# Kernel optimization log

Hardware: AMD Instinct MI355X
Metric: run time of the kernel (lower is better)

Reference implementation:

```python
import jax, jax.numpy as jnp
import numpy as np

N_NODES = 100000
N_EDGES = 1600000
N_FEAT = 16
HEADS = 4


def _feast_conv(x, src, dst, U, c, W, b):
    """FeaStConv: q = softmax_h(u^T(x_j - x_i) + c); out_i = mean_j sum_h q_h * (W_h x_j) + b."""
    n = x.shape[0]
    e = src.shape[0]
    xj = x[src]                                   # [E, Fin] gather
    q = jax.nn.softmax(jnp.matmul(xj - x[dst], U) + c, axis=-1)   # [E, H]
    xs = jnp.matmul(xj, W).reshape(e, HEADS, -1)  # [E, H, Fout]
    msg = jnp.einsum('eh,eho->eo', q, xs)         # [E, Fout]
    deg = jax.ops.segment_sum(jnp.ones((e,), x.dtype), dst, num_segments=n)
    agg = jax.ops.segment_sum(msg, dst, num_segments=n)
    return agg / jnp.maximum(deg, 1.0)[:, None] + b


def setup_inputs() -> dict:
    key = jax.random.key(0)
    ks = jax.random.split(key, 32)
    s = 0.1
    d = {
        'x': jax.random.normal(ks[0], (N_NODES, N_FEAT), jnp.float32),
        'edge_index': jax.random.randint(ks[1], (2, N_EDGES), 0, N_NODES, jnp.int32),
        # conv1: 16 -> 16
        'U1': jax.random.normal(ks[2], (N_FEAT, HEADS), jnp.float32) * s,
        'c1': jnp.zeros((HEADS,), jnp.float32),
        'W1': jax.random.normal(ks[3], (N_FEAT, HEADS * 16), jnp.float32) * s,
        'b1': jnp.zeros((16,), jnp.float32),
        # conv2: 16 -> 32
        'U2': jax.random.normal(ks[4], (16, HEADS), jnp.float32) * s,
        'c2': jnp.zeros((HEADS,), jnp.float32),
        'W2': jax.random.normal(ks[5], (16, HEADS * 32), jnp.float32) * s,
        'b2': jnp.zeros((32,), jnp.float32),
        # conv3: 32 -> 64
        'U3': jax.random.normal(ks[6], (32, HEADS), jnp.float32) * s,
        'c3': jnp.zeros((HEADS,), jnp.float32),
        'W3': jax.random.normal(ks[7], (32, HEADS * 64), jnp.float32) * s,
        'b3': jnp.zeros((64,), jnp.float32),
        # linear tail 64->32->16->8->4->1
        'lw1': jax.random.normal(ks[8], (64, 32), jnp.float32) * s,
        'lb1': jnp.zeros((32,), jnp.float32),
        'lw2': jax.random.normal(ks[9], (32, 16), jnp.float32) * s,
        'lb2': jnp.zeros((16,), jnp.float32),
        'lw3': jax.random.normal(ks[10], (16, 8), jnp.float32) * s,
        'lb3': jnp.zeros((8,), jnp.float32),
        'lw4': jax.random.normal(ks[11], (8, 4), jnp.float32) * s,
        'lb4': jnp.zeros((4,), jnp.float32),
        'lw5': jax.random.normal(ks[12], (4, 1), jnp.float32) * s,
        'lb5': jnp.zeros((1,), jnp.float32),
    }
    return d


def reference(x, edge_index, U1, c1, W1, b1, U2, c2, W2, b2, U3, c3, W3, b3,
              lw1, lb1, lw2, lb2, lw3, lb3, lw4, lb4, lw5, lb5):
    src, dst = edge_index[0], edge_index[1]
    h = jax.nn.relu(_feast_conv(x, src, dst, U1, c1, W1, b1))
    h = jax.nn.relu(_feast_conv(h, src, dst, U2, c2, W2, b2))
    h = jax.nn.relu(_feast_conv(h, src, dst, U3, c3, W3, b3))
    # dropout disabled (inference / drop_bool=False): Linear+ReLU tail
    h = jax.nn.relu(jnp.matmul(h, lw1) + lb1)
    h = jax.nn.relu(jnp.matmul(h, lw2) + lb2)
    h = jax.nn.relu(jnp.matmul(h, lw3) + lb3)
    h = jax.nn.relu(jnp.matmul(h, lw4) + lb4)
    return jax.nn.sigmoid(jnp.matmul(h, lw5) + lb5)   # [N, 1]
```

## Files before the change

### kernel.cpp

```cpp
#include <hip/hip_runtime.h>
#include <math.h>

#define N_NODES 100000
#define N_EDGES 1600000
#define HEADS 4
#define NBKT ((N_NODES + 255) / 256)
#define CHUNK_E 4096
#define NCHUNK ((N_EDGES + CHUNK_E - 1) / CHUNK_E)
#define GN ((N_NODES + 255) / 256)
#define SUM_ROWS 16
#define NRB ((NCHUNK + SUM_ROWS - 1) / SUM_ROWS)

typedef unsigned short ushort_t;
typedef unsigned char  uchar_t;

__device__ __forceinline__ ushort_t f2bf(float x) {
    unsigned u = __float_as_uint(x);
    u += 0x7FFF + ((u >> 16) & 1);
    return (ushort_t)(u >> 16);
}
__device__ __forceinline__ float bf2f(ushort_t v) {
    return __uint_as_float(((unsigned)v) << 16);
}
__device__ __forceinline__ void unpack2(unsigned u, float& lo, float& hi) {
    lo = __uint_as_float(u << 16);
    hi = __uint_as_float(u & 0xffff0000u);
}
__device__ __forceinline__ uchar_t f2fp8(float x) {
    if (x <= 0.0f) return 0;
    unsigned u = __float_as_uint(x) + (1u << 19);
    int e = (int)(u >> 23) - 127 + 15;
    if (e <= 0) return 0;
    if (e > 31) return (uchar_t)255;
    return (uchar_t)((e << 3) | ((u >> 20) & 7));
}
__device__ __forceinline__ float fp8d(uchar_t b) {
    unsigned v = (((unsigned)(b >> 3) + 112u) << 23) | ((unsigned)(b & 7) << 20);
    return (b == 0) ? 0.0f : __uint_as_float(v);
}


__global__ __launch_bounds__(256) void bhist_pcast_kernel(
        const int* __restrict__ dst, int* __restrict__ hist_rows,
        const float* __restrict__ x, const float* __restrict__ U,
        float* __restrict__ p, ushort_t* __restrict__ xbf,
        int* __restrict__ bucket_cnt)
{
    __shared__ int h[NBKT];
    if (blockIdx.x < NCHUNK) {
        for (int i = threadIdx.x; i < NBKT; i += 256) h[i] = 0;
        __syncthreads();
        int base = blockIdx.x * CHUNK_E;
        #pragma unroll
        for (int j = 0; j < CHUNK_E / 256; j++) {
            int e = base + j * 256 + threadIdx.x;
            if (e < N_EDGES) atomicAdd(&h[dst[e] >> 8], 1);
        }
        __syncthreads();
        for (int i = threadIdx.x; i < NBKT; i += 256)
            hist_rows[(size_t)blockIdx.x * NBKT + i] = h[i];
    } else if (blockIdx.x < NCHUNK + GN) {
        int n = (blockIdx.x - NCHUNK) * 256 + threadIdx.x;
        if (n >= N_NODES) return;
        float a0 = 0, a1 = 0, a2 = 0, a3 = 0;
        const float* hr = x + (size_t)n * 16;
        float xv[16];
        #pragma unroll
        for (int f = 0; f < 16; f++) {
            xv[f] = hr[f];
            a0 += xv[f] * U[f * 4 + 0];
            a1 += xv[f] * U[f * 4 + 1];
            a2 += xv[f] * U[f * 4 + 2];
            a3 += xv[f] * U[f * 4 + 3];
        }
        *(float4*)(p + (size_t)n * 4) =
            make_float4(__expf(a0), __expf(a1), __expf(a2), __expf(a3));
        #pragma unroll
        for (int j = 0; j < 4; j++) {
            ushort4 u;
            u.x = f2bf(xv[4 * j + 0]); u.y = f2bf(xv[4 * j + 1]);
            u.z = f2bf(xv[4 * j + 2]); u.w = f2bf(xv[4 * j + 3]);
            *(ushort4*)(xbf + (size_t)n * 16 + 4 * j) = u;
        }
    } else {
        for (int i = threadIdx.x; i < NBKT; i += 256) bucket_cnt[i] = 0;
    }
}


__global__ __launch_bounds__(256) void ksum_kernel(const int* __restrict__ hist_rows,
                                                   int* __restrict__ bucket_cnt) {
    int r0 = blockIdx.x * SUM_ROWS;
    int r1 = min(r0 + SUM_ROWS, NCHUNK);
    for (int i = threadIdx.x; i < NBKT; i += 256) {
        int v = 0;
        for (int r = r0; r < r1; r++) v += hist_rows[(size_t)r * NBKT + i];
        if (v) atomicAdd(&bucket_cnt[i], v);
    }
}


__global__ __launch_bounds__(512) void bscan_kernel(const int* __restrict__ bucket_cnt,
                                                    int* __restrict__ bucket_base,
                                                    int* __restrict__ bucket_cursor) {
    __shared__ int tmp[512];
    int i = threadIdx.x;
    int v = (i < NBKT) ? bucket_cnt[i] : 0;
    tmp[i] = v;
    __syncthreads();
    for (int off = 1; off < 512; off <<= 1) {
        int t = (i >= off) ? tmp[i - off] : 0;
        __syncthreads();
        tmp[i] += t;
        __syncthreads();
    }
    int excl = tmp[i] - v;
    if (i < NBKT) { bucket_base[i] = excl; bucket_cursor[i] = excl; }
    if (i == NBKT) bucket_base[NBKT] = N_EDGES;
}


__global__ __launch_bounds__(256) void partition_kernel(const int* __restrict__ src,
                                                        const int* __restrict__ dst,
                                                        int* __restrict__ bucket_cursor,
                                                        int* __restrict__ csr_tmp) {
    constexpr int EPT = CHUNK_E / 256;
    __shared__ int h[NBKT];
    __shared__ int gbase[NBKT];
    __shared__ int rcnt[NBKT];
    for (int i = threadIdx.x; i < NBKT; i += 256) { h[i] = 0; rcnt[i] = 0; }
    __syncthreads();
    int base = blockIdx.x * CHUNK_E;
    int d[EPT], s[EPT];
    #pragma unroll
    for (int j = 0; j < EPT; j++) {
        int e = base + j * 256 + threadIdx.x;
        d[j] = (e < N_EDGES) ? dst[e] : -1;
        s[j] = (e < N_EDGES) ? src[e] : 0;
        if (d[j] >= 0) atomicAdd(&h[d[j] >> 8], 1);
    }
    __syncthreads();
    for (int i = threadIdx.x; i < NBKT; i += 256)
        if (h[i]) gbase[i] = atomicAdd(&bucket_cursor[i], h[i]);
    __syncthreads();
    #pragma unroll
    for (int j = 0; j < EPT; j++) {
        if (d[j] >= 0) {
            int b = d[j] >> 8;
            int r = atomicAdd(&rcnt[b], 1);
            csr_tmp[gbase[b] + r] = ((d[j] & 255) << 20) | s[j];
        }
    }
}


__global__ __launch_bounds__(256) void bucket_build_kernel(const int* __restrict__ bucket_base,
                                                           const int* __restrict__ csr_tmp,
                                                           int* __restrict__ rowptr,
                                                           int* __restrict__ csr_src) {
    __shared__ int cnt[256];
    __shared__ int tscan[256];
    __shared__ int exc[256];
    __shared__ int stage[8192];
    int b = blockIdx.x;
    int rbeg = bucket_base[b], rend = bucket_base[b + 1];
    int sz = rend - rbeg;
    int tid = threadIdx.x;

    cnt[tid] = 0;
    __syncthreads();
    for (int k = rbeg + tid; k < rend; k += 256) atomicAdd(&cnt[csr_tmp[k] >> 20], 1);
    __syncthreads();
    int v = cnt[tid];
    tscan[tid] = v;
    __syncthreads();
    for (int off = 1; off < 256; off <<= 1) {
        int t = (tid >= off) ? tscan[tid - off] : 0;
        __syncthreads();
        tscan[tid] += t;
        __syncthreads();
    }
    int ex = tscan[tid] - v;
    int node = b * 256 + tid;
    if (node < N_NODES) rowptr[node] = rbeg + ex;
    if (b == 0 && tid == 0) rowptr[N_NODES] = N_EDGES;
    exc[tid] = ex;
    cnt[tid] = 0;
    __syncthreads();

    if (sz <= 8192) {
        for (int k = rbeg + tid; k < rend; k += 256) {
            int pk = csr_tmp[k];
            int dl = pk >> 20;
            int r  = atomicAdd(&cnt[dl], 1);
            stage[exc[dl] + r] = pk;
        }
        __syncthreads();
        for (int i = tid; i < sz; i += 256) csr_src[rbeg + i] = stage[i];
    } else {
        for (int k = rbeg + tid; k < rend; k += 256) {
            int pk = csr_tmp[k];
            int dl = pk >> 20;
            int r  = atomicAdd(&cnt[dl], 1);
            csr_src[rbeg + exc[dl] + r] = pk;
        }
    }
}


template<int FIN, int FOUT, int OUT_FP8>
__global__ __launch_bounds__(256) void conv_fused_kernel(
        const int* __restrict__ rowptr, const int* __restrict__ csr_src,
        const float* __restrict__ es, const float* __restrict__ cvec,
        const ushort_t* __restrict__ hprev,
        const float* __restrict__ W,
        const float* __restrict__ b,
        ushort_t* __restrict__ out_bf,
        uchar_t* __restrict__ out_f8,
        const float* __restrict__ Unext,
        float* __restrict__ esnext)
{
    constexpr int LPN   = FIN / 4;
    constexpr int NPB   = 256 / LPN;
    constexpr int CHUNK = 1024;
    constexpr int K     = 4 * FIN;
    constexpr int ZK    = K + 4;
    constexpr int HS    = FOUT + 1;
    constexpr int WSZ   = K * FOUT;
    constexpr int UNION_A = CHUNK * 16 + CHUNK * 4;
    constexpr int UNION_B = NPB * ZK * 4 + NPB * HS * 4;
    constexpr int UNION   = UNION_A > UNION_B ? UNION_A : UNION_B;

    __shared__ int    sbeg[NPB + 1];
    __shared__ __align__(16) float4 pds[NPB];
    __shared__ __align__(16) float  Ws[WSZ];
    __shared__ float  Uloc[FOUT * 4];
    __shared__ __align__(16) char ubuf[UNION];
    float4* qs    = (float4*)ubuf;
    int*    ssrc  = (int*)(ubuf + CHUNK * 16);
    float*  ztile = (float*)ubuf;
    float*  hout  = (float*)(ubuf + NPB * ZK * 4);

    int tid  = threadIdx.x;
    int nloc = tid / LPN;
    int fl   = (tid - nloc * LPN) * 4;
    int n0   = blockIdx.x * NPB;
    int dbase = n0 & 255;

    float ec0 = __expf(cvec[0]), ec1 = __expf(cvec[1]);
    float ec2 = __expf(cvec[2]), ec3 = __expf(cvec[3]);

    for (int i = tid; i <= NPB; i += 256) {
        int idx = n0 + i;
        sbeg[i] = rowptr[idx > N_NODES ? N_NODES : idx];
    }
    for (int i = tid; i < NPB; i += 256) {
        int idx = n0 + i;
        float4 e = *(const float4*)(es + (size_t)(idx < N_NODES ? idx : N_NODES - 1) * 4);
        pds[i] = make_float4(ec0 / e.x, ec1 / e.y, ec2 / e.z, ec3 / e.w);
    }
    for (int i = tid; i < WSZ; i += 256) {
        int f = i / (4 * FOUT);
        int r = i - f * (4 * FOUT);
        int h = r / FOUT;
        int o = r - h * FOUT;
        Ws[(h * FIN + f) * FOUT + o] = W[i];
    }
    for (int i = tid; i < FOUT * 4; i += 256) Uloc[i] = Unext[i];
    __syncthreads();

    int BB = sbeg[0], BE = sbeg[NPB];
    int beg = sbeg[nloc], end = sbeg[nloc + 1];

    float4 acc0 = make_float4(0, 0, 0, 0), acc1 = acc0, acc2 = acc0, acc3 = acc0;

    for (int cbase = BB; cbase < BE; cbase += CHUNK) {
        int cend = min(cbase + CHUNK, BE);
        __syncthreads();
        for (int k = cbase + tid; k < cend; k += 256) {
            int pk = csr_src[k];
            int s  = pk & ((1 << 20) - 1);
            int nl = (pk >> 20) - dbase;
            float4 e  = *(const float4*)(es + (size_t)s * 4);
            float4 ed = pds[nl];
            float w0 = e.x * ed.x;
            float w1 = e.y * ed.y;
            float w2 = e.z * ed.z;
            float w3 = e.w * ed.w;
            float deg = (float)(sbeg[nl + 1] - sbeg[nl]);
            float inv = 1.0f / (fmaxf(deg, 1.0f) * (w0 + w1 + w2 + w3));
            qs[k - cbase]   = make_float4(w0 * inv, w1 * inv, w2 * inv, w3 * inv);
            ssrc[k - cbase] = s;
        }
        __syncthreads();
        int kb = (beg > cbase ? beg : cbase) - cbase;
        int ke = (end < cend ? end : cend) - cbase;
        int k = kb;
        for (; k + 4 <= ke; k += 4) {
            uint2 r[4];
            #pragma unroll
            for (int j = 0; j < 4; j++)
                r[j] = *(const uint2*)(hprev + (size_t)ssrc[k + j] * FIN + fl);
            float xv[4][4];
            #pragma unroll
            for (int j = 0; j < 4; j++) {
                unpack2(r[j].x, xv[j][0], xv[j][1]);
                unpack2(r[j].y, xv[j][2], xv[j][3]);
            }
            #pragma unroll
            for (int j = 0; j < 4; j++) {
                float4 q = qs[k + j];
                acc0.x += q.x * xv[j][0]; acc0.y += q.x * xv[j][1];
                acc0.z += q.x * xv[j][2]; acc0.w += q.x * xv[j][3];
                acc1.x += q.y * xv[j][0]; acc1.y += q.y * xv[j][1];
                acc1.z += q.y * xv[j][2]; acc1.w += q.y * xv[j][3];
                acc2.x += q.z * xv[j][0]; acc2.y += q.z * xv[j][1];
                acc2.z += q.z * xv[j][2]; acc2.w += q.z * xv[j][3];
                acc3.x += q.w * xv[j][0]; acc3.y += q.w * xv[j][1];
                acc3.z += q.w * xv[j][2]; acc3.w += q.w * xv[j][3];
            }
        }
        for (; k < ke; k++) {
            float x0, x1, x2, x3;
            uint2 r = *(const uint2*)(hprev + (size_t)ssrc[k] * FIN + fl);
            unpack2(r.x, x0, x1);
            unpack2(r.y, x2, x3);
            float4 q = qs[k];
            acc0.x += q.x * x0; acc0.y += q.x * x1; acc0.z += q.x * x2; acc0.w += q.x * x3;
            acc1.x += q.y * x0; acc1.y += q.y * x1; acc1.z += q.y * x2; acc1.w += q.y * x3;
            acc2.x += q.z * x0; acc2.y += q.z * x1; acc2.z += q.z * x2; acc2.w += q.z * x3;
            acc3.x += q.w * x0; acc3.y += q.w * x1; acc3.z += q.w * x2; acc3.w += q.w * x3;
        }
    }

    __syncthreads();
    {
        float* zr = ztile + nloc * ZK;
        *(float4*)(zr + 0 * FIN + fl) = acc0;
        *(float4*)(zr + 1 * FIN + fl) = acc1;
        *(float4*)(zr + 2 * FIN + fl) = acc2;
        *(float4*)(zr + 3 * FIN + fl) = acc3;
    }
    __syncthreads();

    constexpr int OQ  = FOUT / 4;
    constexpr int QPT = (NPB * OQ) / 256;
    #pragma unroll
    for (int rq = 0; rq < QPT; rq++) {
        int idx = tid + 256 * rq;
        int j   = idx / OQ;
        int o4  = idx - j * OQ;
        float4 acc = *(const float4*)(b + 4 * o4);
        const float* zr = ztile + j * ZK;
        #pragma unroll 4
        for (int kq = 0; kq < K / 4; kq++) {
            float4 zt = *(const float4*)(zr + 4 * kq);
            #pragma unroll
            for (int jj = 0; jj < 4; jj++) {
                float4 wv = *(const float4*)(Ws + (4 * kq + jj) * FOUT + 4 * o4);
                float s = (&zt.x)[jj];
                acc.x += s * wv.x;
                acc.y += s * wv.y;
                acc.z += s * wv.z;
                acc.w += s * wv.w;
            }
        }
        acc.x = fmaxf(acc.x, 0.0f);
        acc.y = fmaxf(acc.y, 0.0f);
        acc.z = fmaxf(acc.z, 0.0f);
        acc.w = fmaxf(acc.w, 0.0f);
        float* hr = hout + j * HS + 4 * o4;
        hr[0] = acc.x; hr[1] = acc.y; hr[2] = acc.z; hr[3] = acc.w;
        int nn = n0 + j;
        if (nn < N_NODES) {
            if (OUT_FP8) {
                unsigned pk = (unsigned)f2fp8(acc.x) | ((unsigned)f2fp8(acc.y) << 8) |
                              ((unsigned)f2fp8(acc.z) << 16) | ((unsigned)f2fp8(acc.w) << 24);
                *(unsigned*)(out_f8 + (size_t)nn * FOUT + 4 * o4) = pk;
            } else {
                ushort4 u;
                u.x = f2bf(acc.x); u.y = f2bf(acc.y); u.z = f2bf(acc.z); u.w = f2bf(acc.w);
                *(ushort4*)(out_bf + (size_t)nn * FOUT + 4 * o4) = u;
            }
        }
    }

    __syncthreads();
    if (tid < NPB) {
        int nn = n0 + tid;
        if (nn < N_NODES) {
            float a0 = 0, a1 = 0, a2 = 0, a3 = 0;
            const float* hr = hout + tid * HS;
            #pragma unroll
            for (int ff = 0; ff < FOUT; ff++) {
                float xv = hr[ff];
                a0 += xv * Uloc[ff * 4 + 0];
                a1 += xv * Uloc[ff * 4 + 1];
                a2 += xv * Uloc[ff * 4 + 2];
                a3 += xv * Uloc[ff * 4 + 3];
            }
            *(float4*)(esnext + (size_t)nn * 4) =
                make_float4(__expf(a0), __expf(a1), __expf(a2), __expf(a3));
        }
    }
}


template<int FIN>
__global__ __launch_bounds__(256) void zgather_kernel(
        const int* __restrict__ rowptr, const int* __restrict__ csr_src,
        const float* __restrict__ es, const float* __restrict__ cvec,
        const uchar_t* __restrict__ hf8,
        ushort_t* __restrict__ z)
{
    constexpr int LPN   = FIN / 4;
    constexpr int NPB   = 256 / LPN;
    constexpr int CHUNK = 1024;
    __shared__ int    sbeg[NPB + 1];
    __shared__ __align__(16) float4 pds[NPB];
    __shared__ __align__(16) float4 qs[CHUNK];
    __shared__ int    ssrc[CHUNK];

    int tid  = threadIdx.x;
    int nloc = tid / LPN;
    int fl   = (tid - nloc * LPN) * 4;
    int n0   = blockIdx.x * NPB;
    int n    = n0 + nloc;
    int dbase = n0 & 255;

    float ec0 = __expf(cvec[0]), ec1 = __expf(cvec[1]);
    float ec2 = __expf(cvec[2]), ec3 = __expf(cvec[3]);

    for (int i = tid; i <= NPB; i += 256) {
        int idx = n0 + i;
        sbeg[i] = rowptr[idx > N_NODES ? N_NODES : idx];
    }
    for (int i = tid; i < NPB; i += 256) {
        int idx = n0 + i;
        float4 e = *(const float4*)(es + (size_t)(idx < N_NODES ? idx : N_NODES - 1) * 4);
        pds[i] = make_float4(ec0 / e.x, ec1 / e.y, ec2 / e.z, ec3 / e.w);
    }
    __syncthreads();

    int BB = sbeg[0], BE = sbeg[NPB];
    int beg = sbeg[nloc], end = sbeg[nloc + 1];

    float4 acc0 = make_float4(0, 0, 0, 0), acc1 = acc0, acc2 = acc0, acc3 = acc0;

    for (int cbase = BB; cbase < BE; cbase += CHUNK) {
        int cend = min(cbase + CHUNK, BE);
        __syncthreads();
        for (int k = cbase + tid; k < cend; k += 256) {
            int pk = csr_src[k];
            int s  = pk & ((1 << 20) - 1);
            int nl = (pk >> 20) - dbase;
            float4 e  = *(const float4*)(es + (size_t)s * 4);
            float4 ed = pds[nl];
            float w0 = e.x * ed.x;
            float w1 = e.y * ed.y;
            float w2 = e.z * ed.z;
            float w3 = e.w * ed.w;
            float deg = (float)(sbeg[nl + 1] - sbeg[nl]);
            float inv = 1.0f / (fmaxf(deg, 1.0f) * (w0 + w1 + w2 + w3));
            qs[k - cbase]   = make_float4(w0 * inv, w1 * inv, w2 * inv, w3 * inv);
            ssrc[k - cbase] = s;
        }
        __syncthreads();
        int kb = (beg > cbase ? beg : cbase) - cbase;
        int ke = (end < cend ? end : cend) - cbase;
        int k = kb;
        for (; k + 4 <= ke; k += 4) {
            unsigned r[4];
            #pragma unroll
            for (int j = 0; j < 4; j++)
                r[j] = *(const unsigned*)(hf8 + (size_t)ssrc[k + j] * FIN + fl);
            float xv[4][4];
            #pragma unroll
            for (int j = 0; j < 4; j++) {
                xv[j][0] = fp8d((uchar_t)(r[j] & 255));
                xv[j][1] = fp8d((uchar_t)((r[j] >> 8) & 255));
                xv[j][2] = fp8d((uchar_t)((r[j] >> 16) & 255));
                xv[j][3] = fp8d((uchar_t)(r[j] >> 24));
            }
            #pragma unroll
            for (int j = 0; j < 4; j++) {
                float4 q = qs[k + j];
                acc0.x += q.x * xv[j][0]; acc0.y += q.x * xv[j][1];
                acc0.z += q.x * xv[j][2]; acc0.w += q.x * xv[j][3];
                acc1.x += q.y * xv[j][0]; acc1.y += q.y * xv[j][1];
                acc1.z += q.y * xv[j][2]; acc1.w += q.y * xv[j][3];
                acc2.x += q.z * xv[j][0]; acc2.y += q.z * xv[j][1];
                acc2.z += q.z * xv[j][2]; acc2.w += q.z * xv[j][3];
                acc3.x += q.w * xv[j][0]; acc3.y += q.w * xv[j][1];
                acc3.z += q.w * xv[j][2]; acc3.w += q.w * xv[j][3];
            }
        }
        for (; k < ke; k++) {
            unsigned r = *(const unsigned*)(hf8 + (size_t)ssrc[k] * FIN + fl);
            float x0 = fp8d((uchar_t)(r & 255));
            float x1 = fp8d((uchar_t)((r >> 8) & 255));
            float x2 = fp8d((uchar_t)((r >> 16) & 255));
            float x3 = fp8d((uchar_t)(r >> 24));
            float4 q = qs[k];
            acc0.x += q.x * x0; acc0.y += q.x * x1; acc0.z += q.x * x2; acc0.w += q.x * x3;
            acc1.x += q.y * x0; acc1.y += q.y * x1; acc1.z += q.y * x2; acc1.w += q.y * x3;
            acc2.x += q.z * x0; acc2.y += q.z * x1; acc2.z += q.z * x2; acc2.w += q.z * x3;
            acc3.x += q.w * x0; acc3.y += q.w * x1; acc3.z += q.w * x2; acc3.w += q.w * x3;
        }
    }

    if (n < N_NODES) {
        size_t base = (size_t)n * (4 * FIN) + fl;
        ushort4 u;
        u.x = f2bf(acc0.x); u.y = f2bf(acc0.y); u.z = f2bf(acc0.z); u.w = f2bf(acc0.w);
        *(ushort4*)(z + base) = u;
        u.x = f2bf(acc1.x); u.y = f2bf(acc1.y); u.z = f2bf(acc1.z); u.w = f2bf(acc1.w);
        *(ushort4*)(z + base + FIN) = u;
        u.x = f2bf(acc2.x); u.y = f2bf(acc2.y); u.z = f2bf(acc2.z); u.w = f2bf(acc2.w);
        *(ushort4*)(z + base + 2 * FIN) = u;
        u.x = f2bf(acc3.x); u.y = f2bf(acc3.y); u.z = f2bf(acc3.z); u.w = f2bf(acc3.w);
        *(ushort4*)(z + base + 3 * FIN) = u;
    }
}


template<int FIN, int FOUT>
__global__ __launch_bounds__(256, 4) void post_kernel(
        const ushort_t* __restrict__ z,
        const float* __restrict__ W,
        const float* __restrict__ b,
        ushort_t* __restrict__ out_bf)
{
    constexpr int K   = 4 * FIN;
    constexpr int OL  = FOUT / 4;
    constexpr int NPB = 4 * (256 / OL);
    constexpr int WSZ = FIN * 4 * FOUT;
    __shared__ __align__(16) float Wp[WSZ];
    for (int i = threadIdx.x; i < WSZ; i += 256) {
        int f = i / (4 * FOUT);
        int r = i - f * (4 * FOUT);
        int h = r / FOUT;
        int o = r - h * FOUT;
        Wp[(h * FIN + f) * FOUT + o] = W[i];
    }
    __syncthreads();

    int ol = threadIdx.x % OL;
    int g  = threadIdx.x / OL;
    int n0 = blockIdx.x * NPB + g * 4;

    float4 bv = *(const float4*)(b + 4 * ol);
    float4 acc[4];
    const ushort_t* zr[4];
    #pragma unroll
    for (int j = 0; j < 4; j++) {
        acc[j] = make_float4(0.f, 0.f, 0.f, 0.f);
        int nn = n0 + j; if (nn > N_NODES - 1) nn = N_NODES - 1;
        zr[j] = z + (size_t)nn * K;
    }

    #pragma unroll 2
    for (int kq = 0; kq < K / 4; kq++) {
        float zv[4][4];
        #pragma unroll
        for (int j = 0; j < 4; j++) {
            ushort4 zu = *(const ushort4*)(zr[j] + 4 * kq);
            zv[j][0] = bf2f(zu.x); zv[j][1] = bf2f(zu.y);
            zv[j][2] = bf2f(zu.z); zv[j][3] = bf2f(zu.w);
        }
        #pragma unroll
        for (int jj = 0; jj < 4; jj++) {
            float4 wv = *(const float4*)(Wp + (4 * kq + jj) * FOUT + 4 * ol);
            #pragma unroll
            for (int j = 0; j < 4; j++) {
                float s = zv[j][jj];
                acc[j].x += s * wv.x;
                acc[j].y += s * wv.y;
                acc[j].z += s * wv.z;
                acc[j].w += s * wv.w;
            }
        }
    }

    #pragma unroll
    for (int j = 0; j < 4; j++) {
        int nn = n0 + j;
        if (nn < N_NODES) {
            ushort4 u;
            u.x = f2bf(fmaxf(acc[j].x + bv.x, 0.0f));
            u.y = f2bf(fmaxf(acc[j].y + bv.y, 0.0f));
            u.z = f2bf(fmaxf(acc[j].z + bv.z, 0.0f));
            u.w = f2bf(fmaxf(acc[j].w + bv.w, 0.0f));
            *(ushort4*)(out_bf + (size_t)nn * FOUT + 4 * ol) = u;
        }
    }
}


__global__ __launch_bounds__(256) void tail_kernel(
        const ushort_t* __restrict__ h,
        const float* __restrict__ lw1, const float* __restrict__ lb1,
        const float* __restrict__ lw2, const float* __restrict__ lb2,
        const float* __restrict__ lw3, const float* __restrict__ lb3,
        const float* __restrict__ lw4, const float* __restrict__ lb4,
        const float* __restrict__ lw5, const float* __restrict__ lb5,
        float* __restrict__ out)
{
    __shared__ __align__(16) float w1[64 * 32];
    __shared__ float w2[32 * 16], w3[16 * 8], w4[8 * 4], w5[4];
    __shared__ float B1[32], B2[16], B3[8], B4[4], B5[1];
    for (int i = threadIdx.x; i < 64 * 32; i += blockDim.x) w1[i] = lw1[i];
    for (int i = threadIdx.x; i < 32 * 16; i += blockDim.x) w2[i] = lw2[i];
    for (int i = threadIdx.x; i < 16 * 8;  i += blockDim.x) w3[i] = lw3[i];
    for (int i = threadIdx.x; i < 8 * 4;   i += blockDim.x) w4[i] = lw4[i];
    for (int i = threadIdx.x; i < 4;       i += blockDim.x) w5[i] = lw5[i];
    for (int i = threadIdx.x; i < 32; i += blockDim.x) B1[i] = lb1[i];
    for (int i = threadIdx.x; i < 16; i += blockDim.x) B2[i] = lb2[i];
    for (int i = threadIdx.x; i < 8;  i += blockDim.x) B3[i] = lb3[i];
    for (int i = threadIdx.x; i < 4;  i += blockDim.x) B4[i] = lb4[i];
    if (threadIdx.x == 0) B5[0] = lb5[0];
    __syncthreads();

    int n = blockIdx.x * blockDim.x + threadIdx.x;
    if (n >= N_NODES) return;

    float a[64];
    const uint4* hrow = (const uint4*)(h + (size_t)n * 64);
    #pragma unroll
    for (int j = 0; j < 8; j++) {
        uint4 v = hrow[j];
        unpack2(v.x, a[8 * j + 0], a[8 * j + 1]);
        unpack2(v.y, a[8 * j + 2], a[8 * j + 3]);
        unpack2(v.z, a[8 * j + 4], a[8 * j + 5]);
        unpack2(v.w, a[8 * j + 6], a[8 * j + 7]);
    }

    float t1[32];
    for (int o = 0; o < 32; o++) {
        float acc = B1[o];
        #pragma unroll
        for (int i = 0; i < 64; i++) acc += a[i] * w1[i * 32 + o];
        t1[o] = fmaxf(acc, 0.0f);
    }
    float t2[16];
    for (int o = 0; o < 16; o++) {
        float acc = B2[o];
        #pragma unroll
        for (int i = 0; i < 32; i++) acc += t1[i] * w2[i * 16 + o];
        t2[o] = fmaxf(acc, 0.0f);
    }
    float t3[8];
    for (int o = 0; o < 8; o++) {
        float acc = B3[o];
        #pragma unroll
        for (int i = 0; i < 16; i++) acc += t2[i] * w3[i * 8 + o];
        t3[o] = fmaxf(acc, 0.0f);
    }
    float t4[4];
    for (int o = 0; o < 4; o++) {
        float acc = B4[o];
        #pragma unroll
        for (int i = 0; i < 8; i++) acc += t3[i] * w4[i * 4 + o];
        t4[o] = fmaxf(acc, 0.0f);
    }
    float zf = B5[0];
    #pragma unroll
    for (int i = 0; i < 4; i++) zf += t4[i] * w5[i];
    out[n] = 1.0f / (1.0f + expf(-zf));
}


extern "C" void kernel_launch(void* const* d_in, const int* in_sizes, int n_in,
                              void* d_out, int out_size, void* d_ws, size_t ws_size,
                              hipStream_t stream) {
    const float* x   = (const float*)d_in[0];
    const int*   ei  = (const int*)d_in[1];
    const int*   src = ei;
    const int*   dst = ei + N_EDGES;
    const float* U1 = (const float*)d_in[2];  const float* c1 = (const float*)d_in[3];
    const float* W1 = (const float*)d_in[4];  const float* b1 = (const float*)d_in[5];
    const float* U2 = (const float*)d_in[6];  const float* c2 = (const float*)d_in[7];
    const float* W2 = (const float*)d_in[8];  const float* b2 = (const float*)d_in[9];
    const float* U3 = (const float*)d_in[10]; const float* c3 = (const float*)d_in[11];
    const float* W3 = (const float*)d_in[12]; const float* b3 = (const float*)d_in[13];
    const float* lw1 = (const float*)d_in[14]; const float* lb1 = (const float*)d_in[15];
    const float* lw2 = (const float*)d_in[16]; const float* lb2 = (const float*)d_in[17];
    const float* lw3 = (const float*)d_in[18]; const float* lb3 = (const float*)d_in[19];
    const float* lw4 = (const float*)d_in[20]; const float* lb4 = (const float*)d_in[21];
    const float* lw5 = (const float*)d_in[22]; const float* lb5 = (const float*)d_in[23];

    char* ws = (char*)d_ws;
    size_t off = 0;
    auto alloc = [&](size_t bytes) -> void* {
        void* ptr = (void*)(ws + off);
        off += (bytes + 255) & ~(size_t)255;
        return ptr;
    };
    int*      hist_rows     = (int*)alloc((size_t)NCHUNK * NBKT * 4);
    int*      bucket_cnt    = (int*)alloc((size_t)(NBKT + 1) * 4);
    int*      bucket_base   = (int*)alloc((size_t)(NBKT + 1) * 4);
    int*      bucket_cursor = (int*)alloc((size_t)NBKT * 4);
    int*      csr_tmp       = (int*)alloc((size_t)N_EDGES * 4);
    int*      rowptr        = (int*)alloc(((size_t)N_NODES + 1) * 4);
    int*      csr_src       = (int*)alloc((size_t)N_EDGES * 4);
    float*    p             = (float*)alloc((size_t)N_NODES * 4 * 4);
    ushort_t* z             = (ushort_t*)alloc((size_t)N_NODES * 128 * 2);
    ushort_t* xbf           = (ushort_t*)alloc((size_t)N_NODES * 16 * 2);
    ushort_t* h1bf          = (ushort_t*)alloc((size_t)N_NODES * 16 * 2);
    uchar_t*  h2f8          = (uchar_t*)alloc((size_t)N_NODES * 32);
    ushort_t* h3bf          = (ushort_t*)alloc((size_t)N_NODES * 64 * 2);
    (void)ws_size;
    float* es2 = (float*)z;
    float* es3 = (float*)h3bf;

    const int B = 256;

    bhist_pcast_kernel<<<NCHUNK + GN + 1, B, 0, stream>>>(dst, hist_rows, x, U1, p, xbf,
                                                          bucket_cnt);
    ksum_kernel<<<NRB, B, 0, stream>>>(hist_rows, bucket_cnt);
    bscan_kernel<<<1, 512, 0, stream>>>(bucket_cnt, bucket_base, bucket_cursor);
    partition_kernel<<<NCHUNK, B, 0, stream>>>(src, dst, bucket_cursor, csr_tmp);
    bucket_build_kernel<<<NBKT, B, 0, stream>>>(bucket_base, csr_tmp, rowptr, csr_src);

    const int ZG16 = (N_NODES + 63) / 64;
    const int ZG32 = (N_NODES + 31) / 32;
    const int NPB3 = 4 * (256 / (64 / 4));

    conv_fused_kernel<16, 16, 0><<<ZG16, B, 0, stream>>>(
        rowptr, csr_src, p, c1, xbf, W1, b1, h1bf, nullptr, U2, es2);

    conv_fused_kernel<16, 32, 1><<<ZG16, B, 0, stream>>>(
        rowptr, csr_src, es2, c2, h1bf, W2, b2, nullptr, h2f8, U3, es3);

    zgather_kernel<32><<<ZG32, B, 0, stream>>>(rowptr, csr_src, es3, c3, h2f8, z);
    post_kernel<32, 64><<<(N_NODES + NPB3 - 1) / NPB3, B, 0, stream>>>(z, W3, b3, h3bf);
    tail_kernel<<<GN, B, 0, stream>>>(h3bf, lw1, lb1, lw2, lb2, lw3, lb3,
                                      lw4, lb4, lw5, lb5, (float*)d_out);
}
```

Measured before the change: 322.1 us.

## Pack node features and attention exponents into 64-byte per-node records

Node features (bf16 or fp8) and the per-node exp(u·x) head scores are now interleaved into one 64-byte record per node. Each edge gather touches a single cache line instead of two separate arrays. The per-node es computation moves out of the conv kernel into a separate esnext kernel, which adds two launches and an extra read pass over the records. The gather chunk size is also halved to 512, which lowers LDS use and may allow higher occupancy.

```diff
diff --git a/kernel.cpp b/kernel.cpp
--- a/kernel.cpp
+++ b/kernel.cpp
@@ -40,11 +40,11 @@
 }
 
 
+
 __global__ __launch_bounds__(256) void bhist_pcast_kernel(
         const int* __restrict__ dst, int* __restrict__ hist_rows,
         const float* __restrict__ x, const float* __restrict__ U,
-        float* __restrict__ p, ushort_t* __restrict__ xbf,
-        int* __restrict__ bucket_cnt)
+        char* __restrict__ crec1, int* __restrict__ bucket_cnt)
 {
     __shared__ int h[NBKT];
     if (blockIdx.x < NCHUNK) {
@@ -73,15 +73,16 @@
             a2 += xv[f] * U[f * 4 + 2];
             a3 += xv[f] * U[f * 4 + 3];
         }
-        *(float4*)(p + (size_t)n * 4) =
-            make_float4(__expf(a0), __expf(a1), __expf(a2), __expf(a3));
+        char* rec = crec1 + (size_t)n * 64;
         #pragma unroll
         for (int j = 0; j < 4; j++) {
             ushort4 u;
             u.x = f2bf(xv[4 * j + 0]); u.y = f2bf(xv[4 * j + 1]);
             u.z = f2bf(xv[4 * j + 2]); u.w = f2bf(xv[4 * j + 3]);
-            *(ushort4*)(xbf + (size_t)n * 16 + 4 * j) = u;
-        }
+            *(ushort4*)(rec + 8 * j) = u;
+        }
+        *(float4*)(rec + 32) =
+            make_float4(__expf(a0), __expf(a1), __expf(a2), __expf(a3));
     } else {
         for (int i = threadIdx.x; i < NBKT; i += 256) bucket_cnt[i] = 0;
     }
@@ -211,18 +212,15 @@
 template<int FIN, int FOUT, int OUT_FP8>
 __global__ __launch_bounds__(256) void conv_fused_kernel(
         const int* __restrict__ rowptr, const int* __restrict__ csr_src,
-        const float* __restrict__ es, const float* __restrict__ cvec,
-        const ushort_t* __restrict__ hprev,
+        const char* __restrict__ crec_in,
+        const float* __restrict__ cvec,
         const float* __restrict__ W,
         const float* __restrict__ b,
-        ushort_t* __restrict__ out_bf,
-        uchar_t* __restrict__ out_f8,
-        const float* __restrict__ Unext,
-        float* __restrict__ esnext)
+        char* __restrict__ crec_out)
 {
     constexpr int LPN   = FIN / 4;
     constexpr int NPB   = 256 / LPN;
-    constexpr int CHUNK = 1024;
+    constexpr int CHUNK = 512;
     constexpr int K     = 4 * FIN;
     constexpr int ZK    = K + 4;
     constexpr int HS    = FOUT + 1;
@@ -234,7 +232,6 @@
     __shared__ int    sbeg[NPB + 1];
     __shared__ __align__(16) float4 pds[NPB];
     __shared__ __align__(16) float  Ws[WSZ];
-    __shared__ float  Uloc[FOUT * 4];
     __shared__ __align__(16) char ubuf[UNION];
     float4* qs    = (float4*)ubuf;
     int*    ssrc  = (int*)(ubuf + CHUNK * 16);
@@ -256,7 +253,8 @@
     }
     for (int i = tid; i < NPB; i += 256) {
         int idx = n0 + i;
-        float4 e = *(const float4*)(es + (size_t)(idx < N_NODES ? idx : N_NODES - 1) * 4);
+        float4 e = *(const float4*)(crec_in +
+            (size_t)(idx < N_NODES ? idx : N_NODES - 1) * 64 + 32);
         pds[i] = make_float4(ec0 / e.x, ec1 / e.y, ec2 / e.z, ec3 / e.w);
     }
     for (int i = tid; i < WSZ; i += 256) {
@@ -266,7 +264,6 @@
         int o = r - h * FOUT;
         Ws[(h * FIN + f) * FOUT + o] = W[i];
     }
-    for (int i = tid; i < FOUT * 4; i += 256) Uloc[i] = Unext[i];
     __syncthreads();
 
     int BB = sbeg[0], BE = sbeg[NPB];
@@ -281,7 +278,7 @@
             int pk = csr_src[k];
             int s  = pk & ((1 << 20) - 1);
             int nl = (pk >> 20) - dbase;
-            float4 e  = *(const float4*)(es + (size_t)s * 4);
+            float4 e  = *(const float4*)(crec_in + (size_t)s * 64 + 32);
             float4 ed = pds[nl];
             float w0 = e.x * ed.x;
             float w1 = e.y * ed.y;
@@ -300,7 +297,7 @@
             uint2 r[4];
             #pragma unroll
             for (int j = 0; j < 4; j++)
-                r[j] = *(const uint2*)(hprev + (size_t)ssrc[k + j] * FIN + fl);
+                r[j] = *(const uint2*)(crec_in + (size_t)ssrc[k + j] * 64 + fl * 2);
             float xv[4][4];
             #pragma unroll
             for (int j = 0; j < 4; j++) {
@@ -322,7 +319,7 @@
         }
         for (; k < ke; k++) {
             float x0, x1, x2, x3;
-            uint2 r = *(const uint2*)(hprev + (size_t)ssrc[k] * FIN + fl);
+            uint2 r = *(const uint2*)(crec_in + (size_t)ssrc[k] * 64 + fl * 2);
             unpack2(r.x, x0, x1);
             unpack2(r.y, x2, x3);
             float4 q = qs[k];
@@ -376,11 +373,11 @@
             if (OUT_FP8) {
                 unsigned pk = (unsigned)f2fp8(acc.x) | ((unsigned)f2fp8(acc.y) << 8) |
                               ((unsigned)f2fp8(acc.z) << 16) | ((unsigned)f2fp8(acc.w) << 24);
-                *(unsigned*)(out_f8 + (size_t)nn * FOUT + 4 * o4) = pk;
+                *(unsigned*)(crec_out + (size_t)nn * 64 + 4 * o4) = pk;
             } else {
                 ushort4 u;
                 u.x = f2bf(acc.x); u.y = f2bf(acc.y); u.z = f2bf(acc.z); u.w = f2bf(acc.w);
-                *(ushort4*)(out_bf + (size_t)nn * FOUT + 4 * o4) = u;
+                *(ushort4*)(crec_out + (size_t)nn * 64 + 8 * o4) = u;
             }
         }
     }
@@ -389,33 +386,22 @@
     if (tid < NPB) {
         int nn = n0 + tid;
         if (nn < N_NODES) {
-            float a0 = 0, a1 = 0, a2 = 0, a3 = 0;
-            const float* hr = hout + tid * HS;
-            #pragma unroll
-            for (int ff = 0; ff < FOUT; ff++) {
-                float xv = hr[ff];
-                a0 += xv * Uloc[ff * 4 + 0];
-                a1 += xv * Uloc[ff * 4 + 1];
-                a2 += xv * Uloc[ff * 4 + 2];
-                a3 += xv * Uloc[ff * 4 + 3];
-            }
-            *(float4*)(esnext + (size_t)nn * 4) =
-                make_float4(__expf(a0), __expf(a1), __expf(a2), __expf(a3));
-        }
-    }
-}
+        }
+    }
+}
+
 
 
 template<int FIN>
 __global__ __launch_bounds__(256) void zgather_kernel(
         const int* __restrict__ rowptr, const int* __restrict__ csr_src,
-        const float* __restrict__ es, const float* __restrict__ cvec,
-        const uchar_t* __restrict__ hf8,
+        const char* __restrict__ crec_in,
+        const float* __restrict__ cvec,
         ushort_t* __restrict__ z)
 {
     constexpr int LPN   = FIN / 4;
     constexpr int NPB   = 256 / LPN;
-    constexpr int CHUNK = 1024;
+    constexpr int CHUNK = 512;
     __shared__ int    sbeg[NPB + 1];
     __shared__ __align__(16) float4 pds[NPB];
     __shared__ __align__(16) float4 qs[CHUNK];
@@ -437,7 +423,8 @@
     }
     for (int i = tid; i < NPB; i += 256) {
         int idx = n0 + i;
-        float4 e = *(const float4*)(es + (size_t)(idx < N_NODES ? idx : N_NODES - 1) * 4);
+        float4 e = *(const float4*)(crec_in +
+            (size_t)(idx < N_NODES ? idx : N_NODES - 1) * 64 + 32);
         pds[i] = make_float4(ec0 / e.x, ec1 / e.y, ec2 / e.z, ec3 / e.w);
     }
     __syncthreads();
@@ -454,7 +441,7 @@
             int pk = csr_src[k];
             int s  = pk & ((1 << 20) - 1);
             int nl = (pk >> 20) - dbase;
-            float4 e  = *(const float4*)(es + (size_t)s * 4);
+            float4 e  = *(const float4*)(crec_in + (size_t)s * 64 + 32);
             float4 ed = pds[nl];
             float w0 = e.x * ed.x;
             float w1 = e.y * ed.y;
@@ -473,7 +460,7 @@
             unsigned r[4];
             #pragma unroll
             for (int j = 0; j < 4; j++)
-                r[j] = *(const unsigned*)(hf8 + (size_t)ssrc[k + j] * FIN + fl);
+                r[j] = *(const unsigned*)(crec_in + (size_t)ssrc[k + j] * 64 + fl);
             float xv[4][4];
             #pragma unroll
             for (int j = 0; j < 4; j++) {
@@ -496,7 +483,7 @@
             }
         }
         for (; k < ke; k++) {
-            unsigned r = *(const unsigned*)(hf8 + (size_t)ssrc[k] * FIN + fl);
+            unsigned r = *(const unsigned*)(crec_in + (size_t)ssrc[k] * 64 + fl);
             float x0 = fp8d((uchar_t)(r & 255));
             float x1 = fp8d((uchar_t)((r >> 8) & 255));
             float x2 = fp8d((uchar_t)((r >> 16) & 255));
@@ -521,6 +508,54 @@
         u.x = f2bf(acc3.x); u.y = f2bf(acc3.y); u.z = f2bf(acc3.z); u.w = f2bf(acc3.w);
         *(ushort4*)(z + base + 3 * FIN) = u;
     }
+}
+
+
+template<int FOUT, int ROW_FP8>
+__global__ __launch_bounds__(256) void esnext_kernel(
+        const char* __restrict__ crec,
+        const float* __restrict__ Unext,
+        char* __restrict__ crec_es)
+{
+    __shared__ float Uloc[FOUT * 4];
+    for (int i = threadIdx.x; i < FOUT * 4; i += 256) Uloc[i] = Unext[i];
+    __syncthreads();
+    int n = blockIdx.x * 256 + threadIdx.x;
+    if (n >= N_NODES) return;
+    const char* rec = crec + (size_t)n * 64;
+    float a0 = 0, a1 = 0, a2 = 0, a3 = 0;
+    if (ROW_FP8) {
+        #pragma unroll
+        for (int j = 0; j < FOUT / 4; j++) {
+            unsigned r = *(const unsigned*)(rec + 4 * j);
+            #pragma unroll
+            for (int t = 0; t < 4; t++) {
+                float xv = fp8d((uchar_t)((r >> (8 * t)) & 255));
+                int ff = 4 * j + t;
+                a0 += xv * Uloc[ff * 4 + 0];
+                a1 += xv * Uloc[ff * 4 + 1];
+                a2 += xv * Uloc[ff * 4 + 2];
+                a3 += xv * Uloc[ff * 4 + 3];
+            }
+        }
+    } else {
+        #pragma unroll
+        for (int j = 0; j < FOUT / 4; j++) {
+            ushort4 r = *(const ushort4*)(rec + 8 * j);
+            float x0 = bf2f(r.x), x1 = bf2f(r.y), x2 = bf2f(r.z), x3 = bf2f(r.w);
+            int ff = 4 * j;
+            a0 += x0 * Uloc[ff * 4 + 0] + x1 * Uloc[(ff + 1) * 4 + 0] +
+                  x2 * Uloc[(ff + 2) * 4 + 0] + x3 * Uloc[(ff + 3) * 4 + 0];
+            a1 += x0 * Uloc[ff * 4 + 1] + x1 * Uloc[(ff + 1) * 4 + 1] +
+                  x2 * Uloc[(ff + 2) * 4 + 1] + x3 * Uloc[(ff + 3) * 4 + 1];
+            a2 += x0 * Uloc[ff * 4 + 2] + x1 * Uloc[(ff + 1) * 4 + 2] +
+                  x2 * Uloc[(ff + 2) * 4 + 2] + x3 * Uloc[(ff + 3) * 4 + 2];
+            a3 += x0 * Uloc[ff * 4 + 3] + x1 * Uloc[(ff + 1) * 4 + 3] +
+                  x2 * Uloc[(ff + 2) * 4 + 3] + x3 * Uloc[(ff + 3) * 4 + 3];
+        }
+    }
+    *(float4*)(crec_es + (size_t)n * 64 + 32) =
+        make_float4(__expf(a0), __expf(a1), __expf(a2), __expf(a3));
 }
 
 
@@ -703,20 +738,17 @@
     int*      csr_tmp       = (int*)alloc((size_t)N_EDGES * 4);
     int*      rowptr        = (int*)alloc(((size_t)N_NODES + 1) * 4);
     int*      csr_src       = (int*)alloc((size_t)N_EDGES * 4);
-    float*    p             = (float*)alloc((size_t)N_NODES * 4 * 4);
+    char*     crec1         = (char*)alloc((size_t)N_NODES * 64);
+    char*     crec2         = (char*)alloc((size_t)N_NODES * 64);
+    char*     crec3         = (char*)alloc((size_t)N_NODES * 64);
     ushort_t* z             = (ushort_t*)alloc((size_t)N_NODES * 128 * 2);
-    ushort_t* xbf           = (ushort_t*)alloc((size_t)N_NODES * 16 * 2);
-    ushort_t* h1bf          = (ushort_t*)alloc((size_t)N_NODES * 16 * 2);
-    uchar_t*  h2f8          = (uchar_t*)alloc((size_t)N_NODES * 32);
     ushort_t* h3bf          = (ushort_t*)alloc((size_t)N_NODES * 64 * 2);
     (void)ws_size;
-    float* es2 = (float*)z;
-    float* es3 = (float*)h3bf;
 
     const int B = 256;
 
-    bhist_pcast_kernel<<<NCHUNK + GN + 1, B, 0, stream>>>(dst, hist_rows, x, U1, p, xbf,
-                                                          bucket_cnt);
+    bhist_pcast_kernel<<<NCHUNK + GN + 1, B, 0, stream>>>(dst, hist_rows, x, U1,
+                                                          crec1, bucket_cnt);
     ksum_kernel<<<NRB, B, 0, stream>>>(hist_rows, bucket_cnt);
     bscan_kernel<<<1, 512, 0, stream>>>(bucket_cnt, bucket_base, bucket_cursor);
     partition_kernel<<<NCHUNK, B, 0, stream>>>(src, dst, bucket_cursor, csr_tmp);
@@ -727,12 +759,14 @@
     const int NPB3 = 4 * (256 / (64 / 4));
 
     conv_fused_kernel<16, 16, 0><<<ZG16, B, 0, stream>>>(
-        rowptr, csr_src, p, c1, xbf, W1, b1, h1bf, nullptr, U2, es2);
+        rowptr, csr_src, crec1, c1, W1, b1, crec2);
+    esnext_kernel<16, 0><<<GN, B, 0, stream>>>(crec2, U2, crec2);
 
     conv_fused_kernel<16, 32, 1><<<ZG16, B, 0, stream>>>(
-        rowptr, csr_src, es2, c2, h1bf, W2, b2, nullptr, h2f8, U3, es3);
-
-    zgather_kernel<32><<<ZG32, B, 0, stream>>>(rowptr, csr_src, es3, c3, h2f8, z);
+        rowptr, csr_src, crec2, c2, W2, b2, crec3);
+    esnext_kernel<32, 1><<<GN, B, 0, stream>>>(crec3, U3, crec3);
+
+    zgather_kernel<32><<<ZG32, B, 0, stream>>>(rowptr, csr_src, crec3, c3, z);
     post_kernel<32, 64><<<(N_NODES + NPB3 - 1) / NPB3, B, 0, stream>>>(z, W3, b3, h3bf);
     tail_kernel<<<GN, B, 0, stream>>>(h3bf, lw1, lb1, lw2, lb2, lw3, lb3,
                                       lw4, lb4, lw5, lb5, (float*)d_out);
```

Measured after the change: 348.6 us. 1.08x slower.

## Pack node features and softmax exponentials into interleaved 48-byte records staged in LDS

Applied to the files above, without the earlier changes.

Node features (bf16 or fp8, 32 bytes) and the per-node exp(u·x) float4 are now stored together in one 48-byte record per node. During the chunk prepass each edge loads the whole source record once and stages its 32 feature bytes in shared memory, so the accumulate loop reads LDS instead of issuing a second scattered global gather. This is meant to cut random global transactions per edge, but it doubles LDS per chunk, so CHUNK is halved to 512, which means more chunk iterations and barriers. It also reads 32 bytes even for 16-feature bf16 layers.

```diff
diff --git a/kernel.cpp b/kernel.cpp
--- a/kernel.cpp
+++ b/kernel.cpp
@@ -10,6 +10,7 @@
 #define GN ((N_NODES + 255) / 256)
 #define SUM_ROWS 16
 #define NRB ((NCHUNK + SUM_ROWS - 1) / SUM_ROWS)
+#define RSTRIDE 48
 
 typedef unsigned short ushort_t;
 typedef unsigned char  uchar_t;
@@ -43,8 +44,7 @@
 __global__ __launch_bounds__(256) void bhist_pcast_kernel(
         const int* __restrict__ dst, int* __restrict__ hist_rows,
         const float* __restrict__ x, const float* __restrict__ U,
-        float* __restrict__ p, ushort_t* __restrict__ xbf,
-        int* __restrict__ bucket_cnt)
+        char* __restrict__ crec1, int* __restrict__ bucket_cnt)
 {
     __shared__ int h[NBKT];
     if (blockIdx.x < NCHUNK) {
@@ -73,15 +73,16 @@
             a2 += xv[f] * U[f * 4 + 2];
             a3 += xv[f] * U[f * 4 + 3];
         }
-        *(float4*)(p + (size_t)n * 4) =
-            make_float4(__expf(a0), __expf(a1), __expf(a2), __expf(a3));
+        char* rec = crec1 + (size_t)n * RSTRIDE;
         #pragma unroll
         for (int j = 0; j < 4; j++) {
             ushort4 u;
             u.x = f2bf(xv[4 * j + 0]); u.y = f2bf(xv[4 * j + 1]);
             u.z = f2bf(xv[4 * j + 2]); u.w = f2bf(xv[4 * j + 3]);
-            *(ushort4*)(xbf + (size_t)n * 16 + 4 * j) = u;
-        }
+            *(ushort4*)(rec + 8 * j) = u;
+        }
+        *(float4*)(rec + 32) =
+            make_float4(__expf(a0), __expf(a1), __expf(a2), __expf(a3));
     } else {
         for (int i = threadIdx.x; i < NBKT; i += 256) bucket_cnt[i] = 0;
     }
@@ -211,23 +212,21 @@
 template<int FIN, int FOUT, int OUT_FP8>
 __global__ __launch_bounds__(256) void conv_fused_kernel(
         const int* __restrict__ rowptr, const int* __restrict__ csr_src,
-        const float* __restrict__ es, const float* __restrict__ cvec,
-        const ushort_t* __restrict__ hprev,
+        const char* __restrict__ crec_in,
+        const float* __restrict__ cvec,
         const float* __restrict__ W,
         const float* __restrict__ b,
-        ushort_t* __restrict__ out_bf,
-        uchar_t* __restrict__ out_f8,
-        const float* __restrict__ Unext,
-        float* __restrict__ esnext)
+        char* __restrict__ crec_out,
+        const float* __restrict__ Unext)
 {
     constexpr int LPN   = FIN / 4;
     constexpr int NPB   = 256 / LPN;
-    constexpr int CHUNK = 1024;
+    constexpr int CHUNK = 512;
     constexpr int K     = 4 * FIN;
     constexpr int ZK    = K + 4;
     constexpr int HS    = FOUT + 1;
     constexpr int WSZ   = K * FOUT;
-    constexpr int UNION_A = CHUNK * 16 + CHUNK * 4;
+    constexpr int UNION_A = CHUNK * 16 + CHUNK * 32;
     constexpr int UNION_B = NPB * ZK * 4 + NPB * HS * 4;
     constexpr int UNION   = UNION_A > UNION_B ? UNION_A : UNION_B;
 
@@ -237,7 +236,7 @@
     __shared__ float  Uloc[FOUT * 4];
     __shared__ __align__(16) char ubuf[UNION];
     float4* qs    = (float4*)ubuf;
-    int*    ssrc  = (int*)(ubuf + CHUNK * 16);
+    char*   rows  = ubuf + CHUNK * 16;
     float*  ztile = (float*)ubuf;
     float*  hout  = (float*)(ubuf + NPB * ZK * 4);
 
@@ -256,7 +255,8 @@
     }
     for (int i = tid; i < NPB; i += 256) {
         int idx = n0 + i;
-        float4 e = *(const float4*)(es + (size_t)(idx < N_NODES ? idx : N_NODES - 1) * 4);
+        float4 e = *(const float4*)(crec_in +
+            (size_t)(idx < N_NODES ? idx : N_NODES - 1) * RSTRIDE + 32);
         pds[i] = make_float4(ec0 / e.x, ec1 / e.y, ec2 / e.z, ec3 / e.w);
     }
     for (int i = tid; i < WSZ; i += 256) {
@@ -281,7 +281,13 @@
             int pk = csr_src[k];
             int s  = pk & ((1 << 20) - 1);
             int nl = (pk >> 20) - dbase;
-            float4 e  = *(const float4*)(es + (size_t)s * 4);
+            const char* rec = crec_in + (size_t)s * RSTRIDE;
+            uint4 r0 = *(const uint4*)(rec);
+            uint4 r1 = *(const uint4*)(rec + 16);
+            float4 e = *(const float4*)(rec + 32);
+            char* rw = rows + (size_t)(k - cbase) * 32;
+            *(uint4*)(rw)      = r0;
+            *(uint4*)(rw + 16) = r1;
             float4 ed = pds[nl];
             float w0 = e.x * ed.x;
             float w1 = e.y * ed.y;
@@ -289,8 +295,7 @@
             float w3 = e.w * ed.w;
             float deg = (float)(sbeg[nl + 1] - sbeg[nl]);
             float inv = 1.0f / (fmaxf(deg, 1.0f) * (w0 + w1 + w2 + w3));
-            qs[k - cbase]   = make_float4(w0 * inv, w1 * inv, w2 * inv, w3 * inv);
-            ssrc[k - cbase] = s;
+            qs[k - cbase] = make_float4(w0 * inv, w1 * inv, w2 * inv, w3 * inv);
         }
         __syncthreads();
         int kb = (beg > cbase ? beg : cbase) - cbase;
@@ -300,7 +305,7 @@
             uint2 r[4];
             #pragma unroll
             for (int j = 0; j < 4; j++)
-                r[j] = *(const uint2*)(hprev + (size_t)ssrc[k + j] * FIN + fl);
+                r[j] = *(const uint2*)(rows + (size_t)(k + j) * 32 + fl * 2);
             float xv[4][4];
             #pragma unroll
             for (int j = 0; j < 4; j++) {
@@ -322,7 +327,7 @@
         }
         for (; k < ke; k++) {
             float x0, x1, x2, x3;
-            uint2 r = *(const uint2*)(hprev + (size_t)ssrc[k] * FIN + fl);
+            uint2 r = *(const uint2*)(rows + (size_t)k * 32 + fl * 2);
             unpack2(r.x, x0, x1);
             unpack2(r.y, x2, x3);
             float4 q = qs[k];
@@ -376,11 +381,11 @@
             if (OUT_FP8) {
                 unsigned pk = (unsigned)f2fp8(acc.x) | ((unsigned)f2fp8(acc.y) << 8) |
                               ((unsigned)f2fp8(acc.z) << 16) | ((unsigned)f2fp8(acc.w) << 24);
-                *(unsigned*)(out_f8 + (size_t)nn * FOUT + 4 * o4) = pk;
+                *(unsigned*)(crec_out + (size_t)nn * RSTRIDE + 4 * o4) = pk;
             } else {
                 ushort4 u;
                 u.x = f2bf(acc.x); u.y = f2bf(acc.y); u.z = f2bf(acc.z); u.w = f2bf(acc.w);
-                *(ushort4*)(out_bf + (size_t)nn * FOUT + 4 * o4) = u;
+                *(ushort4*)(crec_out + (size_t)nn * RSTRIDE + 8 * o4) = u;
             }
         }
     }
@@ -399,7 +404,7 @@
                 a2 += xv * Uloc[ff * 4 + 2];
                 a3 += xv * Uloc[ff * 4 + 3];
             }
-            *(float4*)(esnext + (size_t)nn * 4) =
+            *(float4*)(crec_out + (size_t)nn * RSTRIDE + 32) =
                 make_float4(__expf(a0), __expf(a1), __expf(a2), __expf(a3));
         }
     }
@@ -409,17 +414,17 @@
 template<int FIN>
 __global__ __launch_bounds__(256) void zgather_kernel(
         const int* __restrict__ rowptr, const int* __restrict__ csr_src,
-        const float* __restrict__ es, const float* __restrict__ cvec,
-        const uchar_t* __restrict__ hf8,
+        const char* __restrict__ crec_in,
+        const float* __restrict__ cvec,
         ushort_t* __restrict__ z)
 {
     constexpr int LPN   = FIN / 4;
     constexpr int NPB   = 256 / LPN;
-    constexpr int CHUNK = 1024;
+    constexpr int CHUNK = 512;
     __shared__ int    sbeg[NPB + 1];
     __shared__ __align__(16) float4 pds[NPB];
     __shared__ __align__(16) float4 qs[CHUNK];
-    __shared__ int    ssrc[CHUNK];
+    __shared__ __align__(16) char   rows[CHUNK * 32];
 
     int tid  = threadIdx.x;
     int nloc = tid / LPN;
@@ -437,7 +442,8 @@
     }
     for (int i = tid; i < NPB; i += 256) {
         int idx = n0 + i;
-        float4 e = *(const float4*)(es + (size_t)(idx < N_NODES ? idx : N_NODES - 1) * 4);
+        float4 e = *(const float4*)(crec_in +
+            (size_t)(idx < N_NODES ? idx : N_NODES - 1) * RSTRIDE + 32);
         pds[i] = make_float4(ec0 / e.x, ec1 / e.y, ec2 / e.z, ec3 / e.w);
     }
     __syncthreads();
@@ -454,7 +460,13 @@
             int pk = csr_src[k];
             int s  = pk & ((1 << 20) - 1);
             int nl = (pk >> 20) - dbase;
-            float4 e  = *(const float4*)(es + (size_t)s * 4);
+            const char* rec = crec_in + (size_t)s * RSTRIDE;
+            uint4 r0 = *(const uint4*)(rec);
+            uint4 r1 = *(const uint4*)(rec + 16);
+            float4 e = *(const float4*)(rec + 32);
+            char* rw = rows + (size_t)(k - cbase) * 32;
+            *(uint4*)(rw)      = r0;
+            *(uint4*)(rw + 16) = r1;
             float4 ed = pds[nl];
             float w0 = e.x * ed.x;
             float w1 = e.y * ed.y;
@@ -462,8 +474,7 @@
             float w3 = e.w * ed.w;
             float deg = (float)(sbeg[nl + 1] - sbeg[nl]);
             float inv = 1.0f / (fmaxf(deg, 1.0f) * (w0 + w1 + w2 + w3));
-            qs[k - cbase]   = make_float4(w0 * inv, w1 * inv, w2 * inv, w3 * inv);
-            ssrc[k - cbase] = s;
+            qs[k - cbase] = make_float4(w0 * inv, w1 * inv, w2 * inv, w3 * inv);
         }
         __syncthreads();
         int kb = (beg > cbase ? beg : cbase) - cbase;
@@ -473,7 +484,7 @@
             unsigned r[4];
             #pragma unroll
             for (int j = 0; j < 4; j++)
-                r[j] = *(const unsigned*)(hf8 + (size_t)ssrc[k + j] * FIN + fl);
+                r[j] = *(const unsigned*)(rows + (size_t)(k + j) * 32 + fl);
             float xv[4][4];
             #pragma unroll
             for (int j = 0; j < 4; j++) {
@@ -496,7 +507,7 @@
             }
         }
         for (; k < ke; k++) {
-            unsigned r = *(const unsigned*)(hf8 + (size_t)ssrc[k] * FIN + fl);
+            unsigned r = *(const unsigned*)(rows + (size_t)k * 32 + fl);
             float x0 = fp8d((uchar_t)(r & 255));
             float x1 = fp8d((uchar_t)((r >> 8) & 255));
             float x2 = fp8d((uchar_t)((r >> 16) & 255));
@@ -703,20 +714,17 @@
     int*      csr_tmp       = (int*)alloc((size_t)N_EDGES * 4);
     int*      rowptr        = (int*)alloc(((size_t)N_NODES + 1) * 4);
     int*      csr_src       = (int*)alloc((size_t)N_EDGES * 4);
-    float*    p             = (float*)alloc((size_t)N_NODES * 4 * 4);
+    char*     crec1         = (char*)alloc((size_t)N_NODES * RSTRIDE);
+    char*     crec2         = (char*)alloc((size_t)N_NODES * RSTRIDE);
+    char*     crec3         = (char*)alloc((size_t)N_NODES * RSTRIDE);
     ushort_t* z             = (ushort_t*)alloc((size_t)N_NODES * 128 * 2);
-    ushort_t* xbf           = (ushort_t*)alloc((size_t)N_NODES * 16 * 2);
-    ushort_t* h1bf          = (ushort_t*)alloc((size_t)N_NODES * 16 * 2);
-    uchar_t*  h2f8          = (uchar_t*)alloc((size_t)N_NODES * 32);
     ushort_t* h3bf          = (ushort_t*)alloc((size_t)N_NODES * 64 * 2);
     (void)ws_size;
-    float* es2 = (float*)z;
-    float* es3 = (float*)h3bf;
 
     const int B = 256;
 
-    bhist_pcast_kernel<<<NCHUNK + GN + 1, B, 0, stream>>>(dst, hist_rows, x, U1, p, xbf,
-                                                          bucket_cnt);
+    bhist_pcast_kernel<<<NCHUNK + GN + 1, B, 0, stream>>>(dst, hist_rows, x, U1,
+                                                          crec1, bucket_cnt);
     ksum_kernel<<<NRB, B, 0, stream>>>(hist_rows, bucket_cnt);
     bscan_kernel<<<1, 512, 0, stream>>>(bucket_cnt, bucket_base, bucket_cursor);
     partition_kernel<<<NCHUNK, B, 0, stream>>>(src, dst, bucket_cursor, csr_tmp);
@@ -727,12 +735,12 @@
     const int NPB3 = 4 * (256 / (64 / 4));
 
     conv_fused_kernel<16, 16, 0><<<ZG16, B, 0, stream>>>(
-        rowptr, csr_src, p, c1, xbf, W1, b1, h1bf, nullptr, U2, es2);
+        rowptr, csr_src, crec1, c1, W1, b1, crec2, U2);
 
     conv_fused_kernel<16, 32, 1><<<ZG16, B, 0, stream>>>(
-        rowptr, csr_src, es2, c2, h1bf, W2, b2, nullptr, h2f8, U3, es3);
-
-    zgather_kernel<32><<<ZG32, B, 0, stream>>>(rowptr, csr_src, es3, c3, h2f8, z);
+        rowptr, csr_src, crec2, c2, W2, b2, crec3, U3);
+
+    zgather_kernel<32><<<ZG32, B, 0, stream>>>(rowptr, csr_src, crec3, c3, z);
     post_kernel<32, 64><<<(N_NODES + NPB3 - 1) / NPB3, B, 0, stream>>>(z, W3, b3, h3bf);
     tail_kernel<<<GN, B, 0, stream>>>(h3bf, lw1, lb1, lw2, lb2, lw3, lb3,
                                       lw4, lb4, lw5, lb5, (float*)d_out);
```

Result: no change. 316.2 us (-1.8%).
